# Performance work log

Hardware: AMD Instinct MI355X
Metric: run time of the kernel (lower is better)

The kernel has to match this reference:

```python
import jax, jax.numpy as jnp
import numpy as np

B, S, D = 16, 1024, 1024
LR = 0.01  # manual SGD step size inside TTT


def setup_inputs() -> dict:
    key = jax.random.key(0)
    ks = jax.random.split(key, 9)
    s = 1.0 / np.sqrt(D)  # nn.Linear default init range
    lin = lambda k: jax.random.uniform(k, (D, D), jnp.float32, -s, s)
    return {
        "x": jax.random.normal(ks[0], (B, S, D), jnp.float32),
        "noise": jax.random.normal(ks[1], (B, S, D), jnp.float32),
        "alpha1": jax.random.normal(ks[2], (D,), jnp.float32),
        "alpha2": jax.random.normal(ks[3], (D,), jnp.float32),
        "W_map": lin(ks[4]),    # TTT.mapping weight (updated online)
        "W_state": lin(ks[5]),  # TTT.State weight
        "W_probe": lin(ks[6]),  # TTT.Probe weight
        "W_p1": lin(ks[7]),     # GatingUnit.proj_1
        "W_p2": lin(ks[8]),     # GatingUnit.proj_2
    }


def reference(x, noise, alpha1, alpha2, W_map, W_state, W_probe, W_p1, W_p2):
    # --- TTT: sequential per-timestep test-time training, expressed as a scan ---
    def ttt(h):
        xs = jnp.swapaxes(h, 0, 1)       # [S, B, D]
        ns = jnp.swapaxes(noise, 0, 1)   # [S, B, D]

        def step(W, inp):
            x_t, n_t = inp                       # [B, D]
            state = x_t @ W_state.T              # State(x_t)
            tv = state + n_t                     # train_view = state + randn
            err = tv @ W.T - state               # mapping(train_view) - label_view
            # d(mse)/dW for y = x W^T, loss = mean(err^2) over B*D elements
            grad = (2.0 / (x_t.shape[0] * x_t.shape[1])) * (err.T @ tv)
            Wn = W - LR * grad                   # manual SGD update
            readout = (x_t @ W_probe.T) @ Wn.T   # mapping(Probe(x_t)) with updated W
            return Wn, readout

        _, outs = jax.lax.scan(step, W_map, (xs, ns))
        return jnp.swapaxes(outs, 0, 1)          # [B, S, D]

    # --- TensorMapperBlock ---
    res = x
    h = jnp.tanh(alpha1 * x)          # VecDyT norm_1
    x1 = ttt(h) + res
    res2 = x1
    h2 = jnp.tanh(alpha2 * x1)        # VecDyT norm_2
    u = jax.nn.gelu(h2 @ W_p1.T, approximate=False)  # torch nn.GELU (exact)
    v = h2 @ W_p2.T
    return u * v + res2
```

## Files before the change

### kernel.cpp

```cpp
#include <hip/hip_runtime.h>
#include <math.h>


typedef __bf16 bf16;
typedef __attribute__((ext_vector_type(8))) __bf16 bf16x8;
typedef __attribute__((ext_vector_type(4))) __bf16 bf16x4;
typedef __attribute__((ext_vector_type(4))) float f32x4;

#define LAM 1.220703125e-6f

enum { M_TV = 0, M_P = 1, M_E0 = 2, M_CT = 3, M_KP = 4, M_OUT = 5, M_U = 6 };

struct GA {
  const bf16* A;  int lda;
  const bf16* B;  int ldb;
  const bf16* A2; int lda2;
  const bf16* B2; int ldb2;
  int K;
  const float* noise;
  const float* xin;
  const float* alpha2;
  const bf16* TVb;
  const bf16* Vb;
  bf16* H2b;
  float* outf;
  bf16* Cb; int ldc;
};

#define GLOAD_LDS16(gp, lp)                                                   \
  __builtin_amdgcn_global_load_lds(                                           \
      (const __attribute__((address_space(1))) unsigned int*)(gp),            \
      (__attribute__((address_space(3))) unsigned int*)(lp), 16, 0, 0)

#define WAIT_BARRIER(N)                                                       \
  do {                                                                        \
    asm volatile("s_waitcnt vmcnt(" #N ")\n\ts_barrier" ::: "memory");        \
    __builtin_amdgcn_sched_barrier(0);                                        \
  } while (0)

__device__ __forceinline__ void stage_tiles(const bf16* __restrict__ Ap, int lda,
                                            const bf16* __restrict__ Bp, int ldb,
                                            int k0, bf16* As, bf16* Bs, int tid) {
#pragma unroll
  for (int rr = 0; rr < 2; ++rr) {
    int c = tid + (rr << 9);
    int row = c >> 2;
    int kb = (c & 3) ^ ((c >> 3) & 3);
    int lbase = ((tid & 448) + (rr << 9)) << 3;
    GLOAD_LDS16(Ap + (size_t)row * lda + k0 + (kb << 3), As + lbase);
    GLOAD_LDS16(Bp + (size_t)row * ldb + k0 + (kb << 3), Bs + lbase);
  }
}

__device__ __forceinline__ void compute_step(const bf16* As, const bf16* Bs,
                                             int wr, int wc, int m, int gsw,
                                             f32x4 acc[8][4]) {
  bf16x8 af[8], bfr[4];
#pragma unroll
  for (int i = 0; i < 8; ++i)
    af[i] = *(const bf16x8*)(As + (wr + i * 16 + m) * 32 + (gsw << 3));
#pragma unroll
  for (int j = 0; j < 4; ++j)
    bfr[j] = *(const bf16x8*)(Bs + (wc + j * 16 + m) * 32 + (gsw << 3));
  __builtin_amdgcn_s_setprio(1);
#pragma unroll
  for (int i = 0; i < 8; ++i) {
#pragma unroll
    for (int j = 0; j < 4; ++j)
      acc[i][j] =
          __builtin_amdgcn_mfma_f32_16x16x32_bf16(af[i], bfr[j], acc[i][j], 0, 0, 0);
  }
  __builtin_amdgcn_s_setprio(0);
}

template <int MODE>
__device__ __forceinline__ void stage_sel(const GA& g, int s, int steps1,
                                          const bf16* A1, const bf16* B1,
                                          const bf16* A2, const bf16* B2,
                                          bf16* Asb, bf16* Bsb, int tid) {
  if constexpr (MODE == M_OUT) {
    if (s >= steps1) {
      stage_tiles(A2, g.lda2, B2, g.ldb2, (s - steps1) << 5, Asb, Bsb, tid);
      return;
    }
  }
  stage_tiles(A1, g.lda, B1, g.ldb, s << 5, Asb, Bsb, tid);
}

template <int MODE>
__global__ __launch_bounds__(512, 2) void gemm_nt(GA g) {
  __shared__ __attribute__((aligned(16))) bf16 As[4][256 * 32];
  __shared__ __attribute__((aligned(16))) bf16 Bs[4][256 * 32];

  const int gx = gridDim.x, gy = gridDim.y;
  const int nwg = gx * gy * (int)gridDim.z;
  int flat = blockIdx.x + gx * (blockIdx.y + gy * blockIdx.z);
  int swz = (flat & 7) * (nwg >> 3) + (flat >> 3);
  const int bx = swz % gx;
  int t1v = swz / gx;
  const int by = t1v % gy;
  const int bz = t1v / gy;

  const int c0 = bx << 8;
  const int r0 = by << 8;
  if constexpr (MODE == M_KP) {
    if (c0 > r0) return;
  }

  size_t zA = 0, zB = 0, zC = 0;
  if constexpr (MODE == M_CT) { zA = (size_t)bz << 10; zB = zA; zC = (size_t)bz << 20; }
  if constexpr (MODE == M_KP) { zA = (size_t)bz << 20; zB = zA; zC = zA; }
  if constexpr (MODE == M_OUT) { zA = (size_t)bz << 20; zB = (size_t)bz << 10; }

  const int tid = threadIdx.x;
  const int lane = tid & 63, wv = tid >> 6;
  const int wr = (wv >> 2) << 7;
  const int wc = (wv & 3) << 6;
  const int m = lane & 15, ko = lane >> 4;
  const int gsw = ko ^ ((m >> 1) & 3);

  f32x4 acc[8][4];
#pragma unroll
  for (int i = 0; i < 8; ++i) {
#pragma unroll
    for (int j = 0; j < 4; ++j) acc[i][j] = (f32x4){0.f, 0.f, 0.f, 0.f};
  }

  int K1 = g.K;
  if constexpr (MODE == M_OUT) K1 = r0 + 256;
  const int steps1 = K1 >> 5;

  const bf16* A1 = g.A + zA + (size_t)r0 * g.lda;
  const bf16* B1 = g.B + zB + (size_t)c0 * g.ldb;
  const bf16* A2 = nullptr;
  const bf16* B2 = nullptr;
  int total = steps1;
  if constexpr (MODE == M_OUT) {
    A2 = g.A2 + zA + (size_t)r0 * g.lda2;
    B2 = g.B2 + zA + (size_t)c0 * g.ldb2;
    total += 32;
  }

  stage_sel<MODE>(g, 0, steps1, A1, B1, A2, B2, As[0], Bs[0], tid);
  stage_sel<MODE>(g, 1, steps1, A1, B1, A2, B2, As[1], Bs[1], tid);

  int s = 0;
  for (; s < total - 2; ++s) {
    const int rn = (s + 2) & 3;
    stage_sel<MODE>(g, s + 2, steps1, A1, B1, A2, B2, As[rn], Bs[rn], tid);
    WAIT_BARRIER(8);
    compute_step(As[s & 3], Bs[s & 3], wr, wc, m, gsw, acc);
  }
  WAIT_BARRIER(4);
  compute_step(As[s & 3], Bs[s & 3], wr, wc, m, gsw, acc);
  ++s;
  WAIT_BARRIER(0);
  compute_step(As[s & 3], Bs[s & 3], wr, wc, m, gsw, acc);

#pragma unroll
  for (int i = 0; i < 8; ++i) {
#pragma unroll
    for (int j = 0; j < 4; ++j) {
      const int gc = c0 + wc + j * 16 + m;
#pragma unroll
      for (int rg = 0; rg < 4; ++rg) {
        const int grl = r0 + wr + i * 16 + ko * 4 + rg;
        float v = acc[i][j][rg];
        if constexpr (MODE == M_TV) {
          int t = grl >> 4, b = grl & 15;
          float tv = v + g.noise[((size_t)b << 20) + ((size_t)t << 10) + gc];
          g.Cb[(size_t)grl * g.ldc + gc] = (bf16)tv;
        } else if constexpr (MODE == M_P) {
          g.Cb[(size_t)grl * g.ldc + gc] = (bf16)v;
        } else if constexpr (MODE == M_CT) {
          g.Cb[zC + (size_t)grl * g.ldc + gc] = (bf16)v;
        } else if constexpr (MODE == M_E0) {
          int t = grl >> 4, b = grl & 15;
          size_t ni = ((size_t)b << 20) + ((size_t)t << 10) + gc;
          float tvv = (float)g.TVb[(size_t)grl * 1024 + gc];
          float e0 = v - (tvv - g.noise[ni]);
          g.Cb[(size_t)grl * g.ldc + gc] = (bf16)e0;
        } else if constexpr (MODE == M_KP) {
          float sv = ((gc >> 4) <= (grl >> 4)) ? (-LAM * v) : 0.0f;
          g.Cb[zC + (size_t)grl * g.ldc + gc] = (bf16)sv;
        } else if constexpr (MODE == M_OUT) {
          int rgl = (bz << 10) + grl;
          int t = rgl >> 4, b = rgl & 15;
          size_t oi = ((size_t)b << 20) + ((size_t)t << 10) + gc;
          float x1 = v + g.xin[oi];
          g.outf[oi] = x1;
          g.H2b[oi] = (bf16)tanhf(g.alpha2[gc] * x1);
        } else if constexpr (MODE == M_U) {
          size_t oi = (size_t)grl * 1024 + gc;
          float u = v;
          float gl = 0.5f * u * (1.0f + erff(u * 0.70710678118654752f));
          g.outf[oi] = gl * (float)g.Vb[oi] + g.outf[oi];
        }
      }
    }
  }
}

__global__ void ew_convert(const float* w0, const float* w1, const float* w2,
                           const float* w3, const float* w4, bf16* dst) {
  int gid = blockIdx.x * 256 + threadIdx.x;
  int i4 = gid << 2;
  int mm = i4 >> 20;
  const float* src = (mm == 0) ? w0 : (mm == 1) ? w1 : (mm == 2) ? w2
                     : (mm == 3) ? w3 : w4;
  int off = i4 & 1048575;
  float4 v = *(const float4*)(src + off);
  bf16x4 o;
  o[0] = (bf16)v.x; o[1] = (bf16)v.y; o[2] = (bf16)v.z; o[3] = (bf16)v.w;
  *(bf16x4*)(dst + i4) = o;
}

__global__ void ew_h1(const float* __restrict__ x, const float* __restrict__ a1,
                      bf16* __restrict__ H) {
  int gid = blockIdx.x * 256 + threadIdx.x;
  int i4 = gid << 2;
  int d = i4 & 1023;
  int t = (i4 >> 10) & 1023;
  int b = i4 >> 20;
  float4 xv = *(const float4*)(x + i4);
  float4 av = *(const float4*)(a1 + d);
  bf16x4 o;
  o[0] = (bf16)tanhf(av.x * xv.x);
  o[1] = (bf16)tanhf(av.y * xv.y);
  o[2] = (bf16)tanhf(av.z * xv.z);
  o[3] = (bf16)tanhf(av.w * xv.w);
  *(bf16x4*)(H + (((size_t)((t << 4) + b)) << 10) + d) = o;
}

__global__ void prefix_s(const bf16* __restrict__ C, bf16* __restrict__ S,
                         const bf16* __restrict__ W0) {
  int gid = blockIdx.x * 256 + threadIdx.x;
  size_t base = (size_t)gid << 2;
  bf16x4 wv = *(const bf16x4*)(W0 + base);
  float w0 = (float)wv[0], w1 = (float)wv[1], w2 = (float)wv[2],
        w3 = (float)wv[3];
  float ac0 = 0.f, ac1 = 0.f, ac2 = 0.f, ac3 = 0.f;
#pragma unroll
  for (int j = 0; j < 16; ++j) {
    size_t off = ((size_t)j << 20) + base;
    bf16x4 c = *(const bf16x4*)(C + off);
    bf16x4 o;
    o[0] = (bf16)(w0 - LAM * ac0);
    o[1] = (bf16)(w1 - LAM * ac1);
    o[2] = (bf16)(w2 - LAM * ac2);
    o[3] = (bf16)(w3 - LAM * ac3);
    *(bf16x4*)(S + off) = o;
    ac0 += (float)c[0]; ac1 += (float)c[1];
    ac2 += (float)c[2]; ac3 += (float)c[3];
  }
}

__global__ __launch_bounds__(256) void tr_e0(const bf16* __restrict__ in,
                                             bf16* __restrict__ out) {
  __shared__ bf16 tile[64][72];
  int c0 = blockIdx.x << 6;
  int r0 = blockIdx.y << 6;
  int tid = threadIdx.x;
  int lr = tid >> 4;
  int lc = (tid & 15) << 2;
#pragma unroll
  for (int ph = 0; ph < 4; ++ph) {
    int row = lr + (ph << 4);
    bf16x4 v = *(const bf16x4*)(in + (size_t)(r0 + row) * 1024 + c0 + lc);
    *(bf16x4*)(&tile[row][lc]) = v;
  }
  __syncthreads();
#pragma unroll
  for (int ph = 0; ph < 4; ++ph) {
    int oc = lr + (ph << 4);
    bf16x4 v;
    v[0] = tile[lc + 0][oc];
    v[1] = tile[lc + 1][oc];
    v[2] = tile[lc + 2][oc];
    v[3] = tile[lc + 3][oc];
    *(bf16x4*)(out + (size_t)(c0 + oc) * 16384 + r0 + lc) = v;
  }
}

extern "C" void kernel_launch(void* const* d_in, const int* in_sizes, int n_in,
                              void* d_out, int out_size, void* d_ws,
                              size_t ws_size, hipStream_t stream) {
  (void)in_sizes; (void)n_in; (void)out_size;
  const float* x = (const float*)d_in[0];
  const float* noise = (const float*)d_in[1];
  const float* a1 = (const float*)d_in[2];
  const float* a2 = (const float*)d_in[3];
  const float* Wmap = (const float*)d_in[4];
  const float* Wst = (const float*)d_in[5];
  const float* Wpr = (const float*)d_in[6];
  const float* Wp1 = (const float*)d_in[7];
  const float* Wp2 = (const float*)d_in[8];
  float* out = (float*)d_out;

  const size_t MB32 = (size_t)16384 * 1024 * 2;
  const size_t NEED = 5 * MB32 + 5 * (size_t)1048576 * 2;
  if (ws_size < NEED) return;

  char* ws = (char*)d_ws;
  bf16* s0 = (bf16*)(ws);
  bf16* s1 = (bf16*)(ws + MB32);
  bf16* s2 = (bf16*)(ws + 2 * MB32);
  bf16* s3 = (bf16*)(ws + 3 * MB32);
  bf16* s4 = (bf16*)(ws + 4 * MB32);
  bf16* Wcat = (bf16*)(ws + 5 * MB32);
  bf16* Wb0 = Wcat;
  bf16* Wsb = Wcat + (1 << 20);
  bf16* Wpb = Wcat + 2 * (1 << 20);
  bf16* W1b = Wcat + 3 * (1 << 20);
  bf16* W2b = Wcat + 4 * (1 << 20);

  ew_convert<<<5120, 256, 0, stream>>>(Wmap, Wst, Wpr, Wp1, Wp2, Wcat);
  ew_h1<<<16384, 256, 0, stream>>>(x, a1, s0);

  {
    GA g{};
    g.A = s0; g.lda = 1024; g.B = Wsb; g.ldb = 1024; g.K = 1024;
    g.noise = noise; g.Cb = s1; g.ldc = 1024;
    gemm_nt<M_TV><<<dim3(4, 64), 512, 0, stream>>>(g);
  }
  {
    GA g{};
    g.A = s0; g.lda = 1024; g.B = Wpb; g.ldb = 1024; g.K = 1024;
    g.Cb = s2; g.ldc = 1024;
    gemm_nt<M_P><<<dim3(4, 64), 512, 0, stream>>>(g);
  }
  {
    GA g{};
    g.A = s1; g.lda = 1024; g.B = Wb0; g.ldb = 1024; g.K = 1024;
    g.noise = noise; g.TVb = s1; g.Cb = s0; g.ldc = 1024;
    gemm_nt<M_E0><<<dim3(4, 64), 512, 0, stream>>>(g);
  }
  tr_e0<<<dim3(16, 256), 256, 0, stream>>>(s0, s3);
  tr_e0<<<dim3(16, 256), 256, 0, stream>>>(s1, s4);

  {
    GA g{};
    g.A = s3; g.lda = 16384; g.B = s4; g.ldb = 16384; g.K = 1024;
    g.Cb = s0; g.ldc = 1024;
    gemm_nt<M_CT><<<dim3(4, 4, 16), 512, 0, stream>>>(g);
  }
  prefix_s<<<1024, 256, 0, stream>>>(s0, s0, Wb0);

  {
    GA g{};
    g.A = s2; g.lda = 1024; g.B = s1; g.ldb = 1024; g.K = 1024;
    g.Cb = s4; g.ldc = 1024;
    gemm_nt<M_KP><<<dim3(4, 4, 16), 512, 0, stream>>>(g);
  }
  {
    GA g{};
    g.A = s4; g.lda = 1024;
    g.B = s3; g.ldb = 16384;
    g.A2 = s2; g.lda2 = 1024;
    g.B2 = s0; g.ldb2 = 1024;
    g.xin = x; g.outf = out;
    g.alpha2 = a2; g.H2b = s1;
    gemm_nt<M_OUT><<<dim3(4, 4, 16), 512, 0, stream>>>(g);
  }

  {
    GA g{};
    g.A = s1; g.lda = 1024; g.B = W2b; g.ldb = 1024; g.K = 1024;
    g.Cb = s0; g.ldc = 1024;
    gemm_nt<M_P><<<dim3(4, 64), 512, 0, stream>>>(g);
  }
  {
    GA g{};
    g.A = s1; g.lda = 1024; g.B = W1b; g.ldb = 1024; g.K = 1024;
    g.Vb = s0; g.outf = out;
    gemm_nt<M_U><<<dim3(4, 64), 512, 0, stream>>>(g);
  }
}
```

Before: 726.2 us.

## Restructure GEMM mainloop into 64-wide K steps with interleaved half-tile staging

The GEMM main loop now processes K in 64-wide steps with double buffering. Each step is split into four quarter phases that interleave global-to-LDS staging of the next step's A and B halves with MFMA work on the current one, and issue finer-grained barriers and vmcnt waits. The transpose kernel now writes per-chunk blocked [16][1024][1024] layouts instead of a long-stride layout, and the CT/OUT GEMMs use ld=1024 with per-z offsets. The aim is better overlap of memory loads with MFMA and better locality for the transposed operands, at the cost of more barriers per step.

```diff
diff --git a/kernel.cpp b/kernel.cpp
--- a/kernel.cpp
+++ b/kernel.cpp
@@ -32,65 +32,70 @@
       (const __attribute__((address_space(1))) unsigned int*)(gp),            \
       (__attribute__((address_space(3))) unsigned int*)(lp), 16, 0, 0)
 
-#define WAIT_BARRIER(N)                                                       \
+#define BAR()                                                                 \
   do {                                                                        \
-    asm volatile("s_waitcnt vmcnt(" #N ")\n\ts_barrier" ::: "memory");        \
+    asm volatile("s_barrier" ::: "memory");                                   \
     __builtin_amdgcn_sched_barrier(0);                                        \
   } while (0)
 
-__device__ __forceinline__ void stage_tiles(const bf16* __restrict__ Ap, int lda,
-                                            const bf16* __restrict__ Bp, int ldb,
-                                            int k0, bf16* As, bf16* Bs, int tid) {
+#define VMCNT4_BAR()                                                          \
+  do {                                                                        \
+    asm volatile("s_waitcnt vmcnt(4)\n\ts_barrier" ::: "memory");             \
+    __builtin_amdgcn_sched_barrier(0);                                        \
+  } while (0)
+
+#define PRIO_MFMA(I0)                                                         \
+  do {                                                                        \
+    __builtin_amdgcn_s_setprio(1);                                            \
+    _Pragma("unroll") for (int i_ = 0; i_ < 4; ++i_) {                        \
+      _Pragma("unroll") for (int j_ = 0; j_ < 4; ++j_) {                      \
+        acc[(I0) + i_][j_] = __builtin_amdgcn_mfma_f32_16x16x32_bf16(         \
+            af[i_], bfr[j_], acc[(I0) + i_][j_], 0, 0, 0);                    \
+      }                                                                       \
+    }                                                                         \
+    __builtin_amdgcn_s_setprio(0);                                            \
+  } while (0)
+
+__device__ __forceinline__ void stage_half(const bf16* __restrict__ Sp, int ld,
+                                           int k0, bf16* Ls, int tid) {
 #pragma unroll
   for (int rr = 0; rr < 2; ++rr) {
     int c = tid + (rr << 9);
     int row = c >> 2;
     int kb = (c & 3) ^ ((c >> 3) & 3);
     int lbase = ((tid & 448) + (rr << 9)) << 3;
-    GLOAD_LDS16(Ap + (size_t)row * lda + k0 + (kb << 3), As + lbase);
-    GLOAD_LDS16(Bp + (size_t)row * ldb + k0 + (kb << 3), Bs + lbase);
-  }
-}
-
-__device__ __forceinline__ void compute_step(const bf16* As, const bf16* Bs,
-                                             int wr, int wc, int m, int gsw,
-                                             f32x4 acc[8][4]) {
-  bf16x8 af[8], bfr[4];
-#pragma unroll
-  for (int i = 0; i < 8; ++i)
-    af[i] = *(const bf16x8*)(As + (wr + i * 16 + m) * 32 + (gsw << 3));
-#pragma unroll
-  for (int j = 0; j < 4; ++j)
-    bfr[j] = *(const bf16x8*)(Bs + (wc + j * 16 + m) * 32 + (gsw << 3));
-  __builtin_amdgcn_s_setprio(1);
-#pragma unroll
-  for (int i = 0; i < 8; ++i) {
-#pragma unroll
-    for (int j = 0; j < 4; ++j)
-      acc[i][j] =
-          __builtin_amdgcn_mfma_f32_16x16x32_bf16(af[i], bfr[j], acc[i][j], 0, 0, 0);
-  }
-  __builtin_amdgcn_s_setprio(0);
+    GLOAD_LDS16(Sp + (size_t)row * ld + k0 + (kb << 3), Ls + lbase);
+  }
 }
 
 template <int MODE>
-__device__ __forceinline__ void stage_sel(const GA& g, int s, int steps1,
+__device__ __forceinline__ void stage_one(const GA& g, int t, int steps1,
                                           const bf16* A1, const bf16* B1,
                                           const bf16* A2, const bf16* B2,
-                                          bf16* Asb, bf16* Bsb, int tid) {
+                                          int mat, int kh, bf16* Ldst, int tid) {
   if constexpr (MODE == M_OUT) {
-    if (s >= steps1) {
-      stage_tiles(A2, g.lda2, B2, g.ldb2, (s - steps1) << 5, Asb, Bsb, tid);
+    if (t >= steps1) {
+      int tt = t - steps1;
+      if (mat) stage_half(B2, g.ldb2, (tt << 6) + (kh << 5), Ldst, tid);
+      else     stage_half(A2, g.lda2, (tt << 6) + (kh << 5), Ldst, tid);
       return;
     }
   }
-  stage_tiles(A1, g.lda, B1, g.ldb, s << 5, Asb, Bsb, tid);
+  if (mat) stage_half(B1, g.ldb, (t << 6) + (kh << 5), Ldst, tid);
+  else     stage_half(A1, g.lda, (t << 6) + (kh << 5), Ldst, tid);
+}
+
+__device__ __forceinline__ void load_f4(const bf16* Lh, int base, int m,
+                                        int gsw, bf16x8 f[4]) {
+#pragma unroll
+  for (int i = 0; i < 4; ++i)
+    f[i] = *(const bf16x8*)(Lh + (base + i * 16 + m) * 32 + (gsw << 3));
 }
 
 template <int MODE>
 __global__ __launch_bounds__(512, 2) void gemm_nt(GA g) {
-  __shared__ __attribute__((aligned(16))) bf16 As[4][256 * 32];
-  __shared__ __attribute__((aligned(16))) bf16 Bs[4][256 * 32];
+  __shared__ __attribute__((aligned(16))) bf16 LA[2][2][256 * 32];
+  __shared__ __attribute__((aligned(16))) bf16 LB[2][2][256 * 32];
 
   const int gx = gridDim.x, gy = gridDim.y;
   const int nwg = gx * gy * (int)gridDim.z;
@@ -108,9 +113,9 @@
   }
 
   size_t zA = 0, zB = 0, zC = 0;
-  if constexpr (MODE == M_CT) { zA = (size_t)bz << 10; zB = zA; zC = (size_t)bz << 20; }
+  if constexpr (MODE == M_CT) { zA = (size_t)bz << 20; zB = zA; zC = zA; }
   if constexpr (MODE == M_KP) { zA = (size_t)bz << 20; zB = zA; zC = zA; }
-  if constexpr (MODE == M_OUT) { zA = (size_t)bz << 20; zB = (size_t)bz << 10; }
+  if constexpr (MODE == M_OUT) { zA = (size_t)bz << 20; zB = (size_t)bz << 20; }
 
   const int tid = threadIdx.x;
   const int lane = tid & 63, wv = tid >> 6;
@@ -128,34 +133,52 @@
 
   int K1 = g.K;
   if constexpr (MODE == M_OUT) K1 = r0 + 256;
-  const int steps1 = K1 >> 5;
+  const int steps1 = K1 >> 6;
 
   const bf16* A1 = g.A + zA + (size_t)r0 * g.lda;
   const bf16* B1 = g.B + zB + (size_t)c0 * g.ldb;
   const bf16* A2 = nullptr;
   const bf16* B2 = nullptr;
-  int total = steps1;
+  int NT = steps1;
   if constexpr (MODE == M_OUT) {
     A2 = g.A2 + zA + (size_t)r0 * g.lda2;
     B2 = g.B2 + zA + (size_t)c0 * g.ldb2;
-    total += 32;
-  }
-
-  stage_sel<MODE>(g, 0, steps1, A1, B1, A2, B2, As[0], Bs[0], tid);
-  stage_sel<MODE>(g, 1, steps1, A1, B1, A2, B2, As[1], Bs[1], tid);
-
-  int s = 0;
-  for (; s < total - 2; ++s) {
-    const int rn = (s + 2) & 3;
-    stage_sel<MODE>(g, s + 2, steps1, A1, B1, A2, B2, As[rn], Bs[rn], tid);
-    WAIT_BARRIER(8);
-    compute_step(As[s & 3], Bs[s & 3], wr, wc, m, gsw, acc);
-  }
-  WAIT_BARRIER(4);
-  compute_step(As[s & 3], Bs[s & 3], wr, wc, m, gsw, acc);
-  ++s;
-  WAIT_BARRIER(0);
-  compute_step(As[s & 3], Bs[s & 3], wr, wc, m, gsw, acc);
+    NT += 16;
+  }
+
+  stage_one<MODE>(g, 0, steps1, A1, B1, A2, B2, 0, 0, &LA[0][0][0], tid);
+  stage_one<MODE>(g, 0, steps1, A1, B1, A2, B2, 1, 0, &LB[0][0][0], tid);
+  stage_one<MODE>(g, 0, steps1, A1, B1, A2, B2, 0, 1, &LA[0][1][0], tid);
+  stage_one<MODE>(g, 0, steps1, A1, B1, A2, B2, 1, 1, &LB[0][1][0], tid);
+  VMCNT4_BAR();
+
+  bf16x8 af[4], bfr[4];
+  for (int t = 0; t < NT; ++t) {
+    const int cur = t & 1, nb = cur ^ 1;
+    const int tn = (t + 1 < NT) ? t + 1 : 0;
+    load_f4(&LB[cur][0][0], wc, m, gsw, bfr);
+    load_f4(&LA[cur][0][0], wr, m, gsw, af);
+    stage_one<MODE>(g, tn, steps1, A1, B1, A2, B2, 0, 0, &LA[nb][0][0], tid);
+    BAR();
+    PRIO_MFMA(0);
+    BAR();
+    load_f4(&LA[cur][0][0], wr + 64, m, gsw, af);
+    stage_one<MODE>(g, tn, steps1, A1, B1, A2, B2, 1, 0, &LB[nb][0][0], tid);
+    VMCNT4_BAR();
+    PRIO_MFMA(4);
+    BAR();
+    load_f4(&LB[cur][1][0], wc, m, gsw, bfr);
+    load_f4(&LA[cur][1][0], wr, m, gsw, af);
+    stage_one<MODE>(g, tn, steps1, A1, B1, A2, B2, 0, 1, &LA[nb][1][0], tid);
+    BAR();
+    PRIO_MFMA(0);
+    BAR();
+    load_f4(&LA[cur][1][0], wr + 64, m, gsw, af);
+    stage_one<MODE>(g, tn, steps1, A1, B1, A2, B2, 1, 1, &LB[nb][1][0], tid);
+    VMCNT4_BAR();
+    PRIO_MFMA(4);
+    BAR();
+  }
 
 #pragma unroll
   for (int i = 0; i < 8; ++i) {
@@ -270,6 +293,7 @@
     *(bf16x4*)(&tile[row][lc]) = v;
   }
   __syncthreads();
+  const size_t cbase = ((size_t)(r0 >> 10) << 20) + (r0 & 1023) + lc;
 #pragma unroll
   for (int ph = 0; ph < 4; ++ph) {
     int oc = lr + (ph << 4);
@@ -278,7 +302,7 @@
     v[1] = tile[lc + 1][oc];
     v[2] = tile[lc + 2][oc];
     v[3] = tile[lc + 3][oc];
-    *(bf16x4*)(out + (size_t)(c0 + oc) * 16384 + r0 + lc) = v;
+    *(bf16x4*)(out + cbase + (size_t)(c0 + oc) * 1024) = v;
   }
 }
 
@@ -340,7 +364,7 @@
 
   {
     GA g{};
-    g.A = s3; g.lda = 16384; g.B = s4; g.ldb = 16384; g.K = 1024;
+    g.A = s3; g.lda = 1024; g.B = s4; g.ldb = 1024; g.K = 1024;
     g.Cb = s0; g.ldc = 1024;
     gemm_nt<M_CT><<<dim3(4, 4, 16), 512, 0, stream>>>(g);
   }
@@ -355,7 +379,7 @@
   {
     GA g{};
     g.A = s4; g.lda = 1024;
-    g.B = s3; g.ldb = 16384;
+    g.B = s3; g.ldb = 1024;
     g.A2 = s2; g.lda2 = 1024;
     g.B2 = s0; g.ldb2 = 1024;
     g.xin = x; g.outf = out;
```

Result: slower. 775.6 us (+6.8%).

## Fuse TV/probe GEMMs, fuse U/V gating GEMMs, and make transposed buffers chunk-contiguous

Applied to the files above, without the earlier changes.

The State and Probe projections become one GEMM over concatenated weights (Wsb and Wpb are adjacent, so the grid doubles in N), with columns split between two outputs. The two gating-unit GEMMs merge into one kernel that stages half of each W1 and W2 tile, passes the V half through LDS and applies GELU*V plus the residual in-kernel. This removes the bf16 V intermediate round trip and a launch. The transpose kernel now writes per-chunk contiguous [1024x1024] blocks so CT and OUT GEMMs use ld=1024 with 1M-element batch strides, improving locality but changing layout assumptions in several places.

```diff
diff --git a/kernel.cpp b/kernel.cpp
--- a/kernel.cpp
+++ b/kernel.cpp
@@ -9,11 +9,12 @@
 
 #define LAM 1.220703125e-6f
 
-enum { M_TV = 0, M_P = 1, M_E0 = 2, M_CT = 3, M_KP = 4, M_OUT = 5, M_U = 6 };
+enum { M_TVP = 0, M_E0 = 1, M_CT = 2, M_KP = 3, M_OUT = 4, M_UV = 5 };
 
 struct GA {
   const bf16* A;  int lda;
   const bf16* B;  int ldb;
+  const bf16* Bb;
   const bf16* A2; int lda2;
   const bf16* B2; int ldb2;
   int K;
@@ -21,10 +22,10 @@
   const float* xin;
   const float* alpha2;
   const bf16* TVb;
-  const bf16* Vb;
   bf16* H2b;
   float* outf;
-  bf16* Cb; int ldc;
+  bf16* Cb;  int ldc;
+  bf16* Cb2;
 };
 
 #define GLOAD_LDS16(gp, lp)                                                   \
@@ -38,18 +39,63 @@
     __builtin_amdgcn_sched_barrier(0);                                        \
   } while (0)
 
-__device__ __forceinline__ void stage_tiles(const bf16* __restrict__ Ap, int lda,
-                                            const bf16* __restrict__ Bp, int ldb,
-                                            int k0, bf16* As, bf16* Bs, int tid) {
+#define BAR()                                                                 \
+  do {                                                                        \
+    asm volatile("s_barrier" ::: "memory");                                   \
+    __builtin_amdgcn_sched_barrier(0);                                        \
+  } while (0)
+
+__device__ __forceinline__ void stage_mat(const bf16* __restrict__ Sp, int ld,
+                                          int k0, bf16* Ls, int tid) {
 #pragma unroll
   for (int rr = 0; rr < 2; ++rr) {
     int c = tid + (rr << 9);
     int row = c >> 2;
     int kb = (c & 3) ^ ((c >> 3) & 3);
     int lbase = ((tid & 448) + (rr << 9)) << 3;
-    GLOAD_LDS16(Ap + (size_t)row * lda + k0 + (kb << 3), As + lbase);
-    GLOAD_LDS16(Bp + (size_t)row * ldb + k0 + (kb << 3), Bs + lbase);
-  }
+    GLOAD_LDS16(Sp + (size_t)row * ld + k0 + (kb << 3), Ls + lbase);
+  }
+}
+
+__device__ __forceinline__ void stage_uvB(const bf16* __restrict__ W1p,
+                                          const bf16* __restrict__ W2p,
+                                          int k0, bf16* Ls, int tid) {
+  {
+    int c = tid;
+    int row = c >> 2;
+    int kb = (c & 3) ^ ((c >> 3) & 3);
+    int lbase = (tid & 448) << 3;
+    GLOAD_LDS16(W1p + (size_t)row * 1024 + k0 + (kb << 3), Ls + lbase);
+  }
+  {
+    int c = tid + 512;
+    int row = (c >> 2) - 128;
+    int kb = (c & 3) ^ ((c >> 3) & 3);
+    int lbase = ((tid & 448) + 512) << 3;
+    GLOAD_LDS16(W2p + (size_t)row * 1024 + k0 + (kb << 3), Ls + lbase);
+  }
+}
+
+template <int MODE>
+__device__ __forceinline__ void stage_sel(const GA& g, int s, int steps1,
+                                          const bf16* A1, const bf16* B1,
+                                          const bf16* B1b, const bf16* A2,
+                                          const bf16* B2, bf16* As, bf16* Bs,
+                                          int tid) {
+  if constexpr (MODE == M_OUT) {
+    if (s >= steps1) {
+      int k0 = (s - steps1) << 5;
+      stage_mat(A2, g.lda2, k0, As, tid);
+      stage_mat(B2, g.ldb2, k0, Bs, tid);
+      return;
+    }
+  }
+  int k0 = s << 5;
+  stage_mat(A1, g.lda, k0, As, tid);
+  if constexpr (MODE == M_UV)
+    stage_uvB(B1, B1b, k0, Bs, tid);
+  else
+    stage_mat(B1, g.ldb, k0, Bs, tid);
 }
 
 __device__ __forceinline__ void compute_step(const bf16* As, const bf16* Bs,
@@ -71,20 +117,6 @@
           __builtin_amdgcn_mfma_f32_16x16x32_bf16(af[i], bfr[j], acc[i][j], 0, 0, 0);
   }
   __builtin_amdgcn_s_setprio(0);
-}
-
-template <int MODE>
-__device__ __forceinline__ void stage_sel(const GA& g, int s, int steps1,
-                                          const bf16* A1, const bf16* B1,
-                                          const bf16* A2, const bf16* B2,
-                                          bf16* Asb, bf16* Bsb, int tid) {
-  if constexpr (MODE == M_OUT) {
-    if (s >= steps1) {
-      stage_tiles(A2, g.lda2, B2, g.ldb2, (s - steps1) << 5, Asb, Bsb, tid);
-      return;
-    }
-  }
-  stage_tiles(A1, g.lda, B1, g.ldb, s << 5, Asb, Bsb, tid);
 }
 
 template <int MODE>
@@ -101,16 +133,16 @@
   const int by = t1v % gy;
   const int bz = t1v / gy;
 
-  const int c0 = bx << 8;
+  const int c0 = (MODE == M_UV) ? (bx << 7) : (bx << 8);
   const int r0 = by << 8;
   if constexpr (MODE == M_KP) {
     if (c0 > r0) return;
   }
 
   size_t zA = 0, zB = 0, zC = 0;
-  if constexpr (MODE == M_CT) { zA = (size_t)bz << 10; zB = zA; zC = (size_t)bz << 20; }
+  if constexpr (MODE == M_CT) { zA = (size_t)bz << 20; zB = zA; zC = zA; }
   if constexpr (MODE == M_KP) { zA = (size_t)bz << 20; zB = zA; zC = zA; }
-  if constexpr (MODE == M_OUT) { zA = (size_t)bz << 20; zB = (size_t)bz << 10; }
+  if constexpr (MODE == M_OUT) { zA = (size_t)bz << 20; zB = (size_t)bz << 20; }
 
   const int tid = threadIdx.x;
   const int lane = tid & 63, wv = tid >> 6;
@@ -132,22 +164,24 @@
 
   const bf16* A1 = g.A + zA + (size_t)r0 * g.lda;
   const bf16* B1 = g.B + zB + (size_t)c0 * g.ldb;
+  const bf16* B1b = nullptr;
   const bf16* A2 = nullptr;
   const bf16* B2 = nullptr;
   int total = steps1;
+  if constexpr (MODE == M_UV) B1b = g.Bb + (size_t)c0 * 1024;
   if constexpr (MODE == M_OUT) {
     A2 = g.A2 + zA + (size_t)r0 * g.lda2;
     B2 = g.B2 + zA + (size_t)c0 * g.ldb2;
     total += 32;
   }
 
-  stage_sel<MODE>(g, 0, steps1, A1, B1, A2, B2, As[0], Bs[0], tid);
-  stage_sel<MODE>(g, 1, steps1, A1, B1, A2, B2, As[1], Bs[1], tid);
+  stage_sel<MODE>(g, 0, steps1, A1, B1, B1b, A2, B2, As[0], Bs[0], tid);
+  stage_sel<MODE>(g, 1, steps1, A1, B1, B1b, A2, B2, As[1], Bs[1], tid);
 
   int s = 0;
   for (; s < total - 2; ++s) {
     const int rn = (s + 2) & 3;
-    stage_sel<MODE>(g, s + 2, steps1, A1, B1, A2, B2, As[rn], Bs[rn], tid);
+    stage_sel<MODE>(g, s + 2, steps1, A1, B1, B1b, A2, B2, As[rn], Bs[rn], tid);
     WAIT_BARRIER(8);
     compute_step(As[s & 3], Bs[s & 3], wr, wc, m, gsw, acc);
   }
@@ -157,6 +191,45 @@
   WAIT_BARRIER(0);
   compute_step(As[s & 3], Bs[s & 3], wr, wc, m, gsw, acc);
 
+  if constexpr (MODE == M_UV) {
+    bf16* vlds = &As[0][0];
+    BAR();
+    if (wc >= 128) {
+#pragma unroll
+      for (int i = 0; i < 8; ++i) {
+#pragma unroll
+        for (int j = 0; j < 4; ++j) {
+          const int cl = (wc - 128) + j * 16 + m;
+#pragma unroll
+          for (int rg = 0; rg < 4; ++rg) {
+            const int rl = wr + i * 16 + ko * 4 + rg;
+            vlds[rl * 136 + cl] = (bf16)acc[i][j][rg];
+          }
+        }
+      }
+    }
+    BAR();
+    if (wc < 128) {
+#pragma unroll
+      for (int i = 0; i < 8; ++i) {
+#pragma unroll
+        for (int j = 0; j < 4; ++j) {
+          const int cl = wc + j * 16 + m;
+#pragma unroll
+          for (int rg = 0; rg < 4; ++rg) {
+            const int rl = wr + i * 16 + ko * 4 + rg;
+            float u = acc[i][j][rg];
+            float vv = (float)vlds[rl * 136 + cl];
+            float gl = 0.5f * u * (1.0f + erff(u * 0.70710678118654752f));
+            size_t oi = (size_t)(r0 + rl) * 1024 + (c0 + cl);
+            g.outf[oi] = gl * vv + g.outf[oi];
+          }
+        }
+      }
+    }
+    return;
+  }
+
 #pragma unroll
   for (int i = 0; i < 8; ++i) {
 #pragma unroll
@@ -166,20 +239,22 @@
       for (int rg = 0; rg < 4; ++rg) {
         const int grl = r0 + wr + i * 16 + ko * 4 + rg;
         float v = acc[i][j][rg];
-        if constexpr (MODE == M_TV) {
-          int t = grl >> 4, b = grl & 15;
-          float tv = v + g.noise[((size_t)b << 20) + ((size_t)t << 10) + gc];
-          g.Cb[(size_t)grl * g.ldc + gc] = (bf16)tv;
-        } else if constexpr (MODE == M_P) {
-          g.Cb[(size_t)grl * g.ldc + gc] = (bf16)v;
-        } else if constexpr (MODE == M_CT) {
-          g.Cb[zC + (size_t)grl * g.ldc + gc] = (bf16)v;
+        if constexpr (MODE == M_TVP) {
+          if (gc < 1024) {
+            int t = grl >> 4, b = grl & 15;
+            float tv = v + g.noise[((size_t)b << 20) + ((size_t)t << 10) + gc];
+            g.Cb[(size_t)grl * g.ldc + gc] = (bf16)tv;
+          } else {
+            g.Cb2[(size_t)grl * 1024 + (gc - 1024)] = (bf16)v;
+          }
         } else if constexpr (MODE == M_E0) {
           int t = grl >> 4, b = grl & 15;
           size_t ni = ((size_t)b << 20) + ((size_t)t << 10) + gc;
           float tvv = (float)g.TVb[(size_t)grl * 1024 + gc];
           float e0 = v - (tvv - g.noise[ni]);
           g.Cb[(size_t)grl * g.ldc + gc] = (bf16)e0;
+        } else if constexpr (MODE == M_CT) {
+          g.Cb[zC + (size_t)grl * g.ldc + gc] = (bf16)v;
         } else if constexpr (MODE == M_KP) {
           float sv = ((gc >> 4) <= (grl >> 4)) ? (-LAM * v) : 0.0f;
           g.Cb[zC + (size_t)grl * g.ldc + gc] = (bf16)sv;
@@ -190,11 +265,6 @@
           float x1 = v + g.xin[oi];
           g.outf[oi] = x1;
           g.H2b[oi] = (bf16)tanhf(g.alpha2[gc] * x1);
-        } else if constexpr (MODE == M_U) {
-          size_t oi = (size_t)grl * 1024 + gc;
-          float u = v;
-          float gl = 0.5f * u * (1.0f + erff(u * 0.70710678118654752f));
-          g.outf[oi] = gl * (float)g.Vb[oi] + g.outf[oi];
         }
       }
     }
@@ -270,6 +340,7 @@
     *(bf16x4*)(&tile[row][lc]) = v;
   }
   __syncthreads();
+  const size_t cbase = ((size_t)(r0 >> 10) << 20) + (r0 & 1023) + lc;
 #pragma unroll
   for (int ph = 0; ph < 4; ++ph) {
     int oc = lr + (ph << 4);
@@ -278,7 +349,7 @@
     v[1] = tile[lc + 1][oc];
     v[2] = tile[lc + 2][oc];
     v[3] = tile[lc + 3][oc];
-    *(bf16x4*)(out + (size_t)(c0 + oc) * 16384 + r0 + lc) = v;
+    *(bf16x4*)(out + cbase + (size_t)(c0 + oc) * 1024) = v;
   }
 }
 
@@ -310,7 +381,6 @@
   bf16* Wcat = (bf16*)(ws + 5 * MB32);
   bf16* Wb0 = Wcat;
   bf16* Wsb = Wcat + (1 << 20);
-  bf16* Wpb = Wcat + 2 * (1 << 20);
   bf16* W1b = Wcat + 3 * (1 << 20);
   bf16* W2b = Wcat + 4 * (1 << 20);
 
@@ -320,14 +390,8 @@
   {
     GA g{};
     g.A = s0; g.lda = 1024; g.B = Wsb; g.ldb = 1024; g.K = 1024;
-    g.noise = noise; g.Cb = s1; g.ldc = 1024;
-    gemm_nt<M_TV><<<dim3(4, 64), 512, 0, stream>>>(g);
-  }
-  {
-    GA g{};
-    g.A = s0; g.lda = 1024; g.B = Wpb; g.ldb = 1024; g.K = 1024;
-    g.Cb = s2; g.ldc = 1024;
-    gemm_nt<M_P><<<dim3(4, 64), 512, 0, stream>>>(g);
+    g.noise = noise; g.Cb = s1; g.ldc = 1024; g.Cb2 = s2;
+    gemm_nt<M_TVP><<<dim3(8, 64), 512, 0, stream>>>(g);
   }
   {
     GA g{};
@@ -340,7 +404,7 @@
 
   {
     GA g{};
-    g.A = s3; g.lda = 16384; g.B = s4; g.ldb = 16384; g.K = 1024;
+    g.A = s3; g.lda = 1024; g.B = s4; g.ldb = 1024; g.K = 1024;
     g.Cb = s0; g.ldc = 1024;
     gemm_nt<M_CT><<<dim3(4, 4, 16), 512, 0, stream>>>(g);
   }
@@ -355,24 +419,18 @@
   {
     GA g{};
     g.A = s4; g.lda = 1024;
-    g.B = s3; g.ldb = 16384;
+    g.B = s3; g.ldb = 1024;
     g.A2 = s2; g.lda2 = 1024;
     g.B2 = s0; g.ldb2 = 1024;
     g.xin = x; g.outf = out;
     g.alpha2 = a2; g.H2b = s1;
     gemm_nt<M_OUT><<<dim3(4, 4, 16), 512, 0, stream>>>(g);
   }
-
-  {
-    GA g{};
-    g.A = s1; g.lda = 1024; g.B = W2b; g.ldb = 1024; g.K = 1024;
-    g.Cb = s0; g.ldc = 1024;
-    gemm_nt<M_P><<<dim3(4, 64), 512, 0, stream>>>(g);
-  }
-  {
-    GA g{};
-    g.A = s1; g.lda = 1024; g.B = W1b; g.ldb = 1024; g.K = 1024;
-    g.Vb = s0; g.outf = out;
-    gemm_nt<M_U><<<dim3(4, 64), 512, 0, stream>>>(g);
-  }
-}
+  {
+    GA g{};
+    g.A = s1; g.lda = 1024;
+    g.B = W1b; g.ldb = 1024; g.Bb = W2b;
+    g.K = 1024; g.outf = out;
+    gemm_nt<M_UV><<<dim3(8, 64), 512, 0, stream>>>(g);
+  }
+}
```

Result: slower. 831.0 us (+14.4%).
